# Kernel optimization log

Hardware: AMD Instinct MI355X
Metric: run time of the kernel (lower is better)

Reference implementation:

```python
import jax, jax.numpy as jnp
import numpy as np

HEAD_SIZE = 64
EPS_GN = 1e-5 * 8 * 8  # GroupNorm eps = 1e-5 * head_size_divisor**2


def rwkv7_scan(w_raw, q, k, v, a, b):
    """RWKV-7 'wind backstepping' linear recurrence.
    Inputs [B,T,H,N]. Per step (matching the CUDA kernel):
      decay = exp(-exp(w_raw)); sa = S @ a; S = S*decay + sa b^T + v k^T; y = S @ q
    State S is [B,H,N_value,N_key]."""
    decay = jnp.exp(-jnp.exp(w_raw))
    B, T, H, N = q.shape
    xs = tuple(jnp.moveaxis(t, 1, 0) for t in (decay, q, k, v, a, b))  # [T,B,H,N]
    S0 = jnp.zeros((B, H, N, N), q.dtype)

    def step(S, inp):
        d, qt, kt, vt, at, bt = inp
        sa = jnp.einsum('bhij,bhj->bhi', S, at)
        S = S * d[:, :, None, :] + sa[..., None] * bt[:, :, None, :] + vt[..., None] * kt[:, :, None, :]
        y = jnp.einsum('bhij,bhj->bhi', S, qt)
        return S, y

    _, ys = jax.lax.scan(step, S0, xs)
    return jnp.moveaxis(ys, 0, 1)  # [B,T,H,N]


def setup_inputs() -> dict:
    key = jax.random.key(0)
    B, T, C, H, N = 4, 960, 2048, 32, 64
    Dw, Da, Dv, Dg = 96, 96, 64, 256
    ks = iter(jax.random.split(key, 40))

    def nrm(shape, s=0.02):
        return jax.random.normal(next(ks), shape, jnp.float32) * s

    def uni(shape):
        return jax.random.uniform(next(ks), shape, jnp.float32)

    return dict(
        x=nrm((B, T, C), 1.0),
        v_first=nrm((B, T, C), 1.0),
        x_r=uni((1, 1, C)), x_w=uni((1, 1, C)), x_k=uni((1, 1, C)),
        x_v=uni((1, 1, C)), x_a=uni((1, 1, C)), x_g=uni((1, 1, C)),
        w0=jnp.linspace(-7.0, -2.0, C, dtype=jnp.float32).reshape(1, 1, C) + 0.5,
        w1=nrm((C, Dw)), w2=nrm((Dw, C)),
        a0=nrm((1, 1, C)), a1=nrm((C, Da)), a2=nrm((Da, C)),
        v0=jnp.ones((1, 1, C), jnp.float32), v1=nrm((C, Dv)), v2=nrm((Dv, C)),
        g1=nrm((C, Dg)), g2=nrm((Dg, C)),
        k_k=jnp.full((1, 1, C), 0.85, jnp.float32),
        k_a=jnp.ones((1, 1, C), jnp.float32),
        r_k=nrm((H, N)),
        Wr=nrm((C, C)), Wk=nrm((C, C)), Wv=nrm((C, C)), Wo=nrm((C, C)),
        ln_w=jnp.ones((C,), jnp.float32), ln_b=jnp.zeros((C,), jnp.float32),
    )


def reference(x, v_first, x_r, x_w, x_k, x_v, x_a, x_g,
              w0, w1, w2, a0, a1, a2, v0, v1, v2, g1, g2,
              k_k, k_a, r_k, Wr, Wk, Wv, Wo, ln_w, ln_b):
    B, T, C = x.shape
    H = C // HEAD_SIZE
    # time_shift: ZeroPad2d((0,0,1,-1)) == shift right by 1 along T with zero at t=0
    x_prev = jnp.pad(x, ((0, 0), (1, 0), (0, 0)))[:, :T]
    xx = x_prev - x
    xr = x + xx * x_r; xw = x + xx * x_w; xk = x + xx * x_k
    xv = x + xx * x_v; xa = x + xx * x_a; xg = x + xx * x_g

    r = xr @ Wr.T
    w = -jax.nn.softplus(-(w0 + jnp.tanh(xw @ w1) @ w2)) - 0.5
    k = xk @ Wk.T
    v = xv @ Wv.T
    # layer_id != 0: residual-value mixing with first layer's value
    v = v + (v_first - v) * jax.nn.sigmoid(v0 + (xv @ v1) @ v2)
    a = jax.nn.sigmoid(a0 + (xa @ a1) @ a2)
    g = jax.nn.sigmoid(xg @ g1) @ g2

    kk = (k * k_k).reshape(B, T, H, HEAD_SIZE)
    kk = kk / jnp.maximum(jnp.linalg.norm(kk, axis=-1, keepdims=True), 1e-12)  # F.normalize
    kk = kk.reshape(B, T, C)
    k = k * (1 + (a - 1) * k_a)

    hs = lambda t: t.reshape(B, T, H, HEAD_SIZE)
    y = rwkv7_scan(hs(w), hs(r), hs(k), hs(v), hs(-kk), hs(kk * a)).reshape(B, T, C)

    # GroupNorm(H groups over C)
    yg = y.reshape(B, T, H, HEAD_SIZE)
    mu = yg.mean(-1, keepdims=True)
    var = yg.var(-1, keepdims=True)
    y = ((yg - mu) / jnp.sqrt(var + EPS_GN)).reshape(B, T, C) * ln_w + ln_b

    y = y + ((hs(r) * hs(k) * r_k).sum(-1, keepdims=True) * hs(v)).reshape(B, T, C)
    return (y * g) @ Wo.T
```

## Files before the change

### kernel.cpp

```cpp
#include <hip/hip_runtime.h>
#include <stdint.h>

#define BDIM 4
#define TDIM 960
#define CDIM 2048
#define HDIM 32
#define NDIM 64
#define BT   (BDIM*TDIM)

typedef unsigned short u16;
typedef __attribute__((ext_vector_type(8))) short short8;
typedef __attribute__((ext_vector_type(4))) float f32x4;

__device__ __forceinline__ float b2f(u16 u){
  union{unsigned int i; float f;}x; x.i=((unsigned int)u)<<16; return x.f;
}
__device__ __forceinline__ u16 f2b(float f){
  union{float f; unsigned int i;}x; x.f=f;
  unsigned int r = x.i + 0x7fffu + ((x.i>>16)&1u);
  return (u16)(r>>16);
}
__device__ __forceinline__ void unpack8(uint4 p, float* o){
  o[0]=b2f((u16)(p.x&0xffff)); o[1]=b2f((u16)(p.x>>16));
  o[2]=b2f((u16)(p.y&0xffff)); o[3]=b2f((u16)(p.y>>16));
  o[4]=b2f((u16)(p.z&0xffff)); o[5]=b2f((u16)(p.z>>16));
  o[6]=b2f((u16)(p.w&0xffff)); o[7]=b2f((u16)(p.w>>16));
}
__device__ __forceinline__ uint4 pack8(const float* o){
  uint4 p;
  p.x = (unsigned)f2b(o[0]) | ((unsigned)f2b(o[1])<<16);
  p.y = (unsigned)f2b(o[2]) | ((unsigned)f2b(o[3])<<16);
  p.z = (unsigned)f2b(o[4]) | ((unsigned)f2b(o[5])<<16);
  p.w = (unsigned)f2b(o[6]) | ((unsigned)f2b(o[7])<<16);
  return p;
}
__device__ __forceinline__ void ld8f(const float* p, float* o){
  float4 a = *(const float4*)p;
  float4 b = *(const float4*)(p+4);
  o[0]=a.x;o[1]=a.y;o[2]=a.z;o[3]=a.w;o[4]=b.x;o[5]=b.y;o[6]=b.z;o[7]=b.w;
}
__device__ __forceinline__ float sigm(float x){ return 1.f/(1.f+expf(-x)); }
__device__ __forceinline__ void stc(float* p, float v){ *p = v; }
__device__ __forceinline__ void stc(u16* p, float v){ *p = f2b(v); }

__global__ __launch_bounds__(256) void cvt_kernel(const float* src, u16* dst){
  size_t i = ((size_t)blockIdx.x*256 + threadIdx.x)*8;
  float v[8]; ld8f(src+i, v);
  *(uint4*)(dst+i) = pack8(v);
}

struct TJob { const float* src; u16* dst; int R, Cs, DR, DC; };
struct TJobs8 { TJob j[8]; };

__global__ __launch_bounds__(256) void transpose_pad_kernel(TJobs8 jobs){
  TJob jb = jobs.j[blockIdx.z];
  int idx = blockIdx.x*256 + threadIdx.x;
  int total = jb.DR*jb.DC;
  if (idx >= total) return;
  int i = idx / jb.DC, k = idx % jb.DC;
  float v = 0.f;
  if (i < jb.Cs && k < jb.R) v = jb.src[(size_t)k*jb.Cs + i];
  jb.dst[idx] = f2b(v);
}

__global__ __launch_bounds__(256) void mix_kernel(
  const float* x,
  const float* cr, const float* cw, const float* ck,
  const float* cv, const float* ca, const float* cg,
  u16* mr, u16* mw, u16* mk, u16* mv, u16* ma, u16* mg)
{
  size_t tid = (size_t)blockIdx.x*256 + threadIdx.x;
  size_t base = tid*8;
  int c = (int)(base % CDIM);
  int row = (int)(base / CDIM);
  int t = row % TDIM;
  float xc[8], xp[8], xx[8], cf[8], o[8];
  ld8f(x+base, xc);
  if (t > 0) {
    ld8f(x+base-CDIM, xp);
  } else {
    for(int j=0;j<8;j++) xp[j]=0.f;
  }
  #pragma unroll
  for(int j=0;j<8;j++) xx[j]=xp[j]-xc[j];
#define DOMIX(CP, OP) do { ld8f(CP+c, cf); \
  _Pragma("unroll") for(int j=0;j<8;j++) o[j]=xc[j]+xx[j]*cf[j]; \
  *(uint4*)(OP+base)=pack8(o); } while(0)
  DOMIX(cr, mr); DOMIX(cw, mw); DOMIX(ck, mk);
  DOMIX(cv, mv); DOMIX(ca, ma); DOMIX(cg, mg);
#undef DOMIX
}

struct GemmJob {
  const u16* A; const u16* Bt; void* C;
  int nbm, nbn, K, lda, ldb, ldc;
};
struct GemmJobs { GemmJob j[4]; };

template<typename TC>
__global__ __launch_bounds__(256, 2) void gemm_bt_kernel(GemmJobs jobs){
  GemmJob jb = jobs.j[blockIdx.z];
  int bm = blockIdx.x % jb.nbm;
  int bn = blockIdx.x / jb.nbm;
  if (bn >= jb.nbn) return;
  __shared__ __attribute__((aligned(16))) u16 As[128*64];
  __shared__ __attribute__((aligned(16))) u16 Bs[128*64];
  int tid = threadIdx.x;
  int wave = tid>>6, lane = tid&63;
  int wr = wave>>1, wc = wave&1;
  f32x4 acc[4][4];
  #pragma unroll
  for(int i=0;i<4;i++)
    #pragma unroll
    for(int j=0;j<4;j++) acc[i][j] = (f32x4){0.f,0.f,0.f,0.f};
  const int rA0 = bm*128;
  const int rB0 = bn*128;
  int srow = (lane>>3);
  int scol = (lane&7)*8;
  for (int k0=0; k0<jb.K; k0+=64){
    #pragma unroll
    for (int it=0; it<4; ++it){
      int rr = wave*32 + it*8;
      const u16* gA = jb.A + (size_t)(rA0 + rr + srow)*jb.lda + (k0 + scol);
      __builtin_amdgcn_global_load_lds((const __attribute__((address_space(1))) void*)gA,
          (__attribute__((address_space(3))) void*)&As[rr*64], 16, 0, 0);
      const u16* gB = jb.Bt + (size_t)(rB0 + rr + srow)*jb.ldb + (k0 + scol);
      __builtin_amdgcn_global_load_lds((const __attribute__((address_space(1))) void*)gB,
          (__attribute__((address_space(3))) void*)&Bs[rr*64], 16, 0, 0);
    }
    __syncthreads();
    #pragma unroll
    for (int kc=0; kc<2; ++kc){
      short8 af[4], bfr[4];
      int ko = kc*32 + (lane>>4)*8;
      #pragma unroll
      for (int mi=0; mi<4; ++mi)
        af[mi] = *(const short8*)&As[(wr*64 + mi*16 + (lane&15))*64 + ko];
      #pragma unroll
      for (int ni=0; ni<4; ++ni)
        bfr[ni] = *(const short8*)&Bs[(wc*64 + ni*16 + (lane&15))*64 + ko];
      #pragma unroll
      for (int mi=0; mi<4; ++mi)
        #pragma unroll
        for (int ni=0; ni<4; ++ni)
          acc[mi][ni] = __builtin_amdgcn_mfma_f32_16x16x32_bf16(af[mi], bfr[ni], acc[mi][ni], 0, 0, 0);
    }
    __syncthreads();
  }
  TC* C = (TC*)jb.C;
  int cn = (lane&15);
  int rq = (lane>>4)*4;
  #pragma unroll
  for (int mi=0; mi<4; ++mi){
    #pragma unroll
    for (int ni=0; ni<4; ++ni){
      int col = rB0 + wc*64 + ni*16 + cn;
      int row = rA0 + wr*64 + mi*16 + rq;
      #pragma unroll
      for (int e=0; e<4; ++e)
        stc(&C[(size_t)(row+e)*jb.ldc + col], acc[mi][ni][e]);
    }
  }
}

__global__ __launch_bounds__(256) void act_kernel(u16* hw, u16* hg){
  int idx = blockIdx.x*256 + threadIdx.x;
  if (blockIdx.z==0){ if (idx < BT*128) hw[idx] = f2b(tanhf(b2f(hw[idx]))); }
  else              { if (idx < BT*256) hg[idx] = f2b(sigm(b2f(hg[idx]))); }
}

__global__ __launch_bounds__(256) void post_kernel(
  const u16* kbuf, const u16* vraw, const float* vfirst,
  const u16* wl, const u16* al, const u16* vl,
  const float* w0, const float* a0, const float* v0,
  const float* kkc, const float* kac,
  float* dout, u16* ks, u16* vs, u16* as_, u16* bs)
{
  int row = blockIdx.x, tid = threadIdx.x;
  int c = tid*8;
  size_t base = (size_t)row*CDIM + c;
  float kf[8], vr[8], vf[8], wlf[8], alf[8], vlf[8], w0f[8], a0f[8], v0f[8], kkf[8], kaf[8];
  unpack8(*(const uint4*)(kbuf+base), kf);
  unpack8(*(const uint4*)(vraw+base), vr);
  ld8f(vfirst+base, vf);
  unpack8(*(const uint4*)(wl+base), wlf);
  unpack8(*(const uint4*)(al+base), alf);
  unpack8(*(const uint4*)(vl+base), vlf);
  ld8f(w0+c, w0f);
  ld8f(a0+c, a0f);
  ld8f(v0+c, v0f);
  ld8f(kkc+c, kkf);
  ld8f(kac+c, kaf);
  float dv[8], av[8], vv[8], kkr[8], kfin[8], asv[8], bsv[8];
  float ssq = 0.f;
  #pragma unroll
  for (int j=0;j<8;j++){
    float wv = -log1pf(expf(-(w0f[j]+wlf[j]))) - 0.5f;
    dv[j]  = expf(-expf(wv));
    av[j]  = sigm(a0f[j]+alf[j]);
    vv[j]  = vr[j] + (vf[j]-vr[j])*sigm(v0f[j]+vlf[j]);
    kkr[j] = kf[j]*kkf[j];
    ssq   += kkr[j]*kkr[j];
    kfin[j]= kf[j]*(1.f + (av[j]-1.f)*kaf[j]);
  }
  ssq += __shfl_xor(ssq,1); ssq += __shfl_xor(ssq,2); ssq += __shfl_xor(ssq,4);
  float inv = 1.f/fmaxf(sqrtf(ssq), 1e-12f);
  #pragma unroll
  for (int j=0;j<8;j++){ float kkn = kkr[j]*inv; asv[j] = -kkn; bsv[j] = kkn*av[j]; }
  *(float4*)(dout+base)   = make_float4(dv[0],dv[1],dv[2],dv[3]);
  *(float4*)(dout+base+4) = make_float4(dv[4],dv[5],dv[6],dv[7]);
  *(uint4*)(ks+base)  = pack8(kfin);
  *(uint4*)(vs+base)  = pack8(vv);
  *(uint4*)(as_+base) = pack8(asv);
  *(uint4*)(bs+base)  = pack8(bsv);
}

__global__ __launch_bounds__(256) void scan_kernel(
  const float* decayp, const u16* qb, const u16* kb, const u16* vb,
  const u16* ab, const u16* bb, float* yb)
{
  const int DEC=0, QQ=512, KK=1024, AA=1536, BB=2048, VV=2560, BUF=2816;
  __shared__ float sb[2*2816];
  int blk = blockIdx.x;
  int b    = blk >> 6;
  int h    = (blk >> 1) & 31;
  int half = blk & 1;
  int tid = threadIdx.x;
  int jg = tid & 7;
  int ii = tid >> 3;
  int row = half*32 + ii;
  int lst = tid >> 5;
  int lc  = tid & 31;
  size_t hbase = ((size_t)b*TDIM)*CDIM + (size_t)h*NDIM;

  float S[8];
  #pragma unroll
  for (int e=0;e<8;e++) S[e]=0.f;

  float2 dreg; unsigned qreg, kreg, areg, breg; u16 vreg;
  auto load_group = [&](int t0){
    size_t g = hbase + (size_t)(t0+lst)*CDIM + lc*2;
    dreg = *(const float2*)(decayp + g);
    qreg = *(const unsigned*)(qb + g);
    kreg = *(const unsigned*)(kb + g);
    areg = *(const unsigned*)(ab + g);
    breg = *(const unsigned*)(bb + g);
    vreg = vb[hbase + (size_t)(t0+lst)*CDIM + half*32 + lc];
  };
  auto store_group = [&](int p){
    float* buf = &sb[p*BUF];
    *(float2*)&buf[DEC + lst*64 + lc*2] = dreg;
    *(float2*)&buf[QQ  + lst*64 + lc*2] = make_float2(b2f((u16)(qreg&0xffff)), b2f((u16)(qreg>>16)));
    *(float2*)&buf[KK  + lst*64 + lc*2] = make_float2(b2f((u16)(kreg&0xffff)), b2f((u16)(kreg>>16)));
    *(float2*)&buf[AA  + lst*64 + lc*2] = make_float2(b2f((u16)(areg&0xffff)), b2f((u16)(areg>>16)));
    *(float2*)&buf[BB  + lst*64 + lc*2] = make_float2(b2f((u16)(breg&0xffff)), b2f((u16)(breg>>16)));
    buf[VV + lst*32 + lc] = b2f(vreg);
  };

  load_group(0);
  store_group(0);
  __syncthreads();
  int p = 0;
  for (int g=0; g<120; ++g){
    if (g+1 < 120) load_group((g+1)*8);
    const float* buf = &sb[p*BUF];
    #pragma unroll
    for (int s=0; s<8; ++s){
      f32x4 a0 = *(const f32x4*)&buf[AA + s*64 + jg*8];
      f32x4 a1 = *(const f32x4*)&buf[AA + s*64 + jg*8 + 4];
      float sap = S[0]*a0[0]+S[1]*a0[1]+S[2]*a0[2]+S[3]*a0[3]
                + S[4]*a1[0]+S[5]*a1[1]+S[6]*a1[2]+S[7]*a1[3];
      sap += __shfl_xor(sap,1);
      sap += __shfl_xor(sap,2);
      sap += __shfl_xor(sap,4);
      f32x4 d0 = *(const f32x4*)&buf[DEC + s*64 + jg*8];
      f32x4 d1 = *(const f32x4*)&buf[DEC + s*64 + jg*8 + 4];
      f32x4 k0 = *(const f32x4*)&buf[KK + s*64 + jg*8];
      f32x4 k1 = *(const f32x4*)&buf[KK + s*64 + jg*8 + 4];
      f32x4 b0 = *(const f32x4*)&buf[BB + s*64 + jg*8];
      f32x4 b1 = *(const f32x4*)&buf[BB + s*64 + jg*8 + 4];
      f32x4 q0 = *(const f32x4*)&buf[QQ + s*64 + jg*8];
      f32x4 q1 = *(const f32x4*)&buf[QQ + s*64 + jg*8 + 4];
      float vi = buf[VV + s*32 + ii];
      float yp = 0.f;
      #pragma unroll
      for (int e=0;e<4;e++){
        S[e]   = S[e]*d0[e]   + sap*b0[e] + vi*k0[e];
        yp    += S[e]*q0[e];
        S[e+4] = S[e+4]*d1[e] + sap*b1[e] + vi*k1[e];
        yp    += S[e+4]*q1[e];
      }
      yp += __shfl_xor(yp,1);
      yp += __shfl_xor(yp,2);
      yp += __shfl_xor(yp,4);
      if (jg==0) yb[hbase + (size_t)(g*8+s)*CDIM + row] = yp;
    }
    if (g+1 < 120) store_group(p^1);
    __syncthreads();
    p ^= 1;
  }
}

__global__ __launch_bounds__(256) void final_kernel(
  const float* yb, const u16* rb, const u16* ks, const u16* vs,
  const float* rk, const float* lnw, const float* lnb, const u16* gl, u16* yg)
{
  int row = blockIdx.x, tid = threadIdx.x;
  int c = tid*8;
  size_t base = (size_t)row*CDIM + c;
  float y[8], rf[8], kf[8], vf[8], rkf[8], lw[8], lb[8], gf[8];
  ld8f(yb+base, y);
  unpack8(*(const uint4*)(rb+base), rf);
  unpack8(*(const uint4*)(ks+base), kf);
  unpack8(*(const uint4*)(vs+base), vf);
  ld8f(rk+c,  rkf);
  ld8f(lnw+c, lw);
  ld8f(lnb+c, lb);
  unpack8(*(const uint4*)(gl+base), gf);
  float sy=0.f, syy=0.f, coef=0.f;
  #pragma unroll
  for (int j=0;j<8;j++){ sy+=y[j]; syy+=y[j]*y[j]; coef += rf[j]*kf[j]*rkf[j]; }
  sy  += __shfl_xor(sy,1);  sy  += __shfl_xor(sy,2);  sy  += __shfl_xor(sy,4);
  syy += __shfl_xor(syy,1); syy += __shfl_xor(syy,2); syy += __shfl_xor(syy,4);
  coef+= __shfl_xor(coef,1);coef+= __shfl_xor(coef,2);coef+= __shfl_xor(coef,4);
  float mu  = sy*(1.f/64.f);
  float var = syy*(1.f/64.f) - mu*mu;
  float rs  = rsqrtf(var + 6.4e-4f);
  float o[8];
  #pragma unroll
  for (int j=0;j<8;j++)
    o[j] = (((y[j]-mu)*rs)*lw[j] + lb[j] + coef*vf[j]) * gf[j];
  *(uint4*)(yg+base) = pack8(o);
}

extern "C" void kernel_launch(void* const* d_in, const int* in_sizes, int n_in,
                              void* d_out, int out_size, void* d_ws, size_t ws_size,
                              hipStream_t stream)
{
  const float* x      = (const float*)d_in[0];
  const float* vfirst = (const float*)d_in[1];
  const float* c_r = (const float*)d_in[2];
  const float* c_w = (const float*)d_in[3];
  const float* c_k = (const float*)d_in[4];
  const float* c_v = (const float*)d_in[5];
  const float* c_a = (const float*)d_in[6];
  const float* c_g = (const float*)d_in[7];
  const float* w0i = (const float*)d_in[8];
  const float* w1i = (const float*)d_in[9];
  const float* w2i = (const float*)d_in[10];
  const float* a0i = (const float*)d_in[11];
  const float* a1i = (const float*)d_in[12];
  const float* a2i = (const float*)d_in[13];
  const float* v0i = (const float*)d_in[14];
  const float* v1i = (const float*)d_in[15];
  const float* v2i = (const float*)d_in[16];
  const float* g1i = (const float*)d_in[17];
  const float* g2i = (const float*)d_in[18];
  const float* kki = (const float*)d_in[19];
  const float* kai = (const float*)d_in[20];
  const float* rki = (const float*)d_in[21];
  const float* Wr  = (const float*)d_in[22];
  const float* Wk  = (const float*)d_in[23];
  const float* Wv  = (const float*)d_in[24];
  const float* Wo  = (const float*)d_in[25];
  const float* lnw = (const float*)d_in[26];
  const float* lnb = (const float*)d_in[27];

  char* ws = (char*)d_ws;
  const size_t S2 = (size_t)BT*CDIM*2;
  u16* MIXR = (u16*)(ws + 0*S2);
  u16* MIXW = (u16*)(ws + 1*S2);
  u16* MIXK = (u16*)(ws + 2*S2);
  u16* MIXV = (u16*)(ws + 3*S2);
  u16* MIXA = (u16*)(ws + 4*S2);
  u16* MIXG = (u16*)(ws + 5*S2);
  u16* RBUF = (u16*)(ws + 6*S2);
  u16* KBUF = (u16*)(ws + 7*S2);
  u16* VRAW = (u16*)(ws + 8*S2);
  char* WB = ws + 9*S2;
  u16* WSLOT = (u16*)WB;
  char* WT = WB + 8388608;
  u16* W1T = (u16*)(WT + 0);
  u16* A1T = (u16*)(WT + 524288);
  u16* V1T = (u16*)(WT + 1048576);
  u16* G1T = (u16*)(WT + 1572864);
  u16* W2T = (u16*)(WT + 2621440);
  u16* A2T = (u16*)(WT + 3145728);
  u16* V2T = (u16*)(WT + 3670016);
  u16* G2T = (u16*)(WT + 4194304);
  char* HB = WT + 5242880;
  u16* HW = (u16*)(HB + 0);
  u16* HA = (u16*)(HB + 983040);
  u16* HV = (u16*)(HB + 1966080);
  u16* HG = (u16*)(HB + 2949120);
  char* L2 = HB + 4915200;
  u16* WL = (u16*)(L2 + 0*S2);
  u16* AL = (u16*)(L2 + 1*S2);
  u16* VL = (u16*)(L2 + 2*S2);
  u16* GL = (u16*)(L2 + 3*S2);
  float* WDEC = (float*)(ws + 0*S2);
  u16* KS = (u16*)(ws + 2*S2);
  u16* VS = (u16*)(ws + 3*S2);
  u16* AS = (u16*)(ws + 4*S2);
  u16* BS = (u16*)(ws + 5*S2);
  float* YBUF = (float*)(L2 + 0*S2);
  u16* YG = (u16*)(L2 + 2*S2);
  (void)in_sizes; (void)n_in; (void)out_size; (void)ws_size;

  TJobs8 tj;
  tj.j[0] = (TJob){w1i, W1T, 2048,  96, 128, 2048};
  tj.j[1] = (TJob){a1i, A1T, 2048,  96, 128, 2048};
  tj.j[2] = (TJob){v1i, V1T, 2048,  64, 128, 2048};
  tj.j[3] = (TJob){g1i, G1T, 2048, 256, 256, 2048};
  tj.j[4] = (TJob){w2i, W2T,   96, 2048, 2048, 128};
  tj.j[5] = (TJob){a2i, A2T,   96, 2048, 2048, 128};
  tj.j[6] = (TJob){v2i, V2T,   64, 2048, 2048, 128};
  tj.j[7] = (TJob){g2i, G2T,  256, 2048, 2048, 256};
  transpose_pad_kernel<<<dim3(2048,1,8), 256, 0, stream>>>(tj);

  mix_kernel<<<dim3(BT*CDIM/8/256), 256, 0, stream>>>(
      x, c_r, c_w, c_k, c_v, c_a, c_g, MIXR, MIXW, MIXK, MIXV, MIXA, MIXG);

  {
    GemmJobs gj;
    cvt_kernel<<<dim3(2048), 256, 0, stream>>>(Wr, WSLOT);
    gj.j[0] = (GemmJob){MIXR, WSLOT, RBUF, 30, 16, 2048, 2048, 2048, 2048};
    gj.j[1] = gj.j[0]; gj.j[2] = gj.j[0]; gj.j[3] = gj.j[0];
    gemm_bt_kernel<u16><<<dim3(480,1,1), 256, 0, stream>>>(gj);
    cvt_kernel<<<dim3(2048), 256, 0, stream>>>(Wk, WSLOT);
    gj.j[0] = (GemmJob){MIXK, WSLOT, KBUF, 30, 16, 2048, 2048, 2048, 2048};
    gemm_bt_kernel<u16><<<dim3(480,1,1), 256, 0, stream>>>(gj);
    cvt_kernel<<<dim3(2048), 256, 0, stream>>>(Wv, WSLOT);
    gj.j[0] = (GemmJob){MIXV, WSLOT, VRAW, 30, 16, 2048, 2048, 2048, 2048};
    gemm_bt_kernel<u16><<<dim3(480,1,1), 256, 0, stream>>>(gj);
  }

  GemmJobs lj1;
  lj1.j[0] = (GemmJob){MIXW, W1T, HW, 30, 1, 2048, 2048, 2048, 128};
  lj1.j[1] = (GemmJob){MIXA, A1T, HA, 30, 1, 2048, 2048, 2048, 128};
  lj1.j[2] = (GemmJob){MIXV, V1T, HV, 30, 1, 2048, 2048, 2048, 128};
  lj1.j[3] = (GemmJob){MIXG, G1T, HG, 30, 2, 2048, 2048, 2048, 256};
  gemm_bt_kernel<u16><<<dim3(60,1,4), 256, 0, stream>>>(lj1);

  act_kernel<<<dim3(3840,1,2), 256, 0, stream>>>(HW, HG);

  GemmJobs lj2;
  lj2.j[0] = (GemmJob){HW, W2T, WL, 30, 16, 128, 128, 128, 2048};
  lj2.j[1] = (GemmJob){HA, A2T, AL, 30, 16, 128, 128, 128, 2048};
  lj2.j[2] = (GemmJob){HV, V2T, VL, 30, 16, 128, 128, 128, 2048};
  lj2.j[3] = (GemmJob){HG, G2T, GL, 30, 16, 256, 256, 256, 2048};
  gemm_bt_kernel<u16><<<dim3(480,1,4), 256, 0, stream>>>(lj2);

  post_kernel<<<dim3(BT), 256, 0, stream>>>(
      KBUF, VRAW, vfirst, WL, AL, VL, w0i, a0i, v0i, kki, kai,
      WDEC, KS, VS, AS, BS);

  scan_kernel<<<dim3(256), 256, 0, stream>>>(
      WDEC, RBUF, KS, VS, AS, BS, YBUF);

  final_kernel<<<dim3(BT), 256, 0, stream>>>(
      YBUF, RBUF, KS, VS, rki, lnw, lnb, GL, YG);

  cvt_kernel<<<dim3(2048), 256, 0, stream>>>(Wo, WSLOT);
  GemmJobs oj;
  oj.j[0] = (GemmJob){YG, WSLOT, d_out, 30, 16, 2048, 2048, 2048, 2048};
  oj.j[1] = oj.j[0]; oj.j[2] = oj.j[0]; oj.j[3] = oj.j[0];
  gemm_bt_kernel<float><<<dim3(480,1,1), 256, 0, stream>>>(oj);
}
```

Before: 908.2 us.

## Split scan state rows into quarters across 512 blocks with deferred y reduction

The RWKV-7 scan is now split four ways over value rows instead of two, giving 512 blocks of 256 threads, each thread holding 4 state elements instead of 8. Each row's dot products use 16 lanes, so the reductions gain an extra shuffle stage. The y reductions for the 8 timesteps in a group are batched after the inner loop, taking them off the serial per-step chain. The aim is more parallelism on a latency-bound recurrence, at the cost of redundantly loading each head's key-side vectors into LDS twice as many times.

```diff
diff --git a/kernel.cpp b/kernel.cpp
--- a/kernel.cpp
+++ b/kernel.cpp
@@ -215,29 +215,30 @@
   *(uint4*)(bs+base)  = pack8(bsv);
 }
 
-__global__ __launch_bounds__(256) void scan_kernel(
+__global__ __launch_bounds__(256, 2) void scan_kernel(
   const float* decayp, const u16* qb, const u16* kb, const u16* vb,
   const u16* ab, const u16* bb, float* yb)
 {
-  const int DEC=0, QQ=512, KK=1024, AA=1536, BB=2048, VV=2560, BUF=2816;
-  __shared__ float sb[2*2816];
+  const int DEC=0, QQ=512, KK=1024, AA=1536, BB=2048, VV=2560, BUF=2688;
+  __shared__ float sb[2*2688];
   int blk = blockIdx.x;
-  int b    = blk >> 6;
-  int h    = (blk >> 1) & 31;
-  int half = blk & 1;
+  int b    = blk >> 7;
+  int h    = (blk >> 2) & 31;
+  int qtr  = blk & 3;
   int tid = threadIdx.x;
-  int jg = tid & 7;
-  int ii = tid >> 3;
-  int row = half*32 + ii;
+  int jg = tid & 15;
+  int ii = tid >> 4;
+  int row0 = qtr*16;
+  int row = row0 + ii;
   int lst = tid >> 5;
   int lc  = tid & 31;
   size_t hbase = ((size_t)b*TDIM)*CDIM + (size_t)h*NDIM;
 
-  float S[8];
-  #pragma unroll
-  for (int e=0;e<8;e++) S[e]=0.f;
-
-  float2 dreg; unsigned qreg, kreg, areg, breg; u16 vreg;
+  float S[4];
+  #pragma unroll
+  for (int e=0;e<4;e++) S[e]=0.f;
+
+  float2 dreg; unsigned qreg, kreg, areg, breg; u16 vreg=0;
   auto load_group = [&](int t0){
     size_t g = hbase + (size_t)(t0+lst)*CDIM + lc*2;
     dreg = *(const float2*)(decayp + g);
@@ -245,7 +246,7 @@
     kreg = *(const unsigned*)(kb + g);
     areg = *(const unsigned*)(ab + g);
     breg = *(const unsigned*)(bb + g);
-    vreg = vb[hbase + (size_t)(t0+lst)*CDIM + half*32 + lc];
+    if (lc < 16) vreg = vb[hbase + (size_t)(t0+lst)*CDIM + row0 + lc];
   };
   auto store_group = [&](int p){
     float* buf = &sb[p*BUF];
@@ -254,7 +255,7 @@
     *(float2*)&buf[KK  + lst*64 + lc*2] = make_float2(b2f((u16)(kreg&0xffff)), b2f((u16)(kreg>>16)));
     *(float2*)&buf[AA  + lst*64 + lc*2] = make_float2(b2f((u16)(areg&0xffff)), b2f((u16)(areg>>16)));
     *(float2*)&buf[BB  + lst*64 + lc*2] = make_float2(b2f((u16)(breg&0xffff)), b2f((u16)(breg>>16)));
-    buf[VV + lst*32 + lc] = b2f(vreg);
+    if (lc < 16) buf[VV + lst*16 + lc] = b2f(vreg);
   };
 
   load_group(0);
@@ -264,36 +265,37 @@
   for (int g=0; g<120; ++g){
     if (g+1 < 120) load_group((g+1)*8);
     const float* buf = &sb[p*BUF];
+    float yp[8];
     #pragma unroll
     for (int s=0; s<8; ++s){
-      f32x4 a0 = *(const f32x4*)&buf[AA + s*64 + jg*8];
-      f32x4 a1 = *(const f32x4*)&buf[AA + s*64 + jg*8 + 4];
-      float sap = S[0]*a0[0]+S[1]*a0[1]+S[2]*a0[2]+S[3]*a0[3]
-                + S[4]*a1[0]+S[5]*a1[1]+S[6]*a1[2]+S[7]*a1[3];
+      f32x4 a0 = *(const f32x4*)&buf[AA + s*64 + jg*4];
+      float sap = (S[0]*a0[0] + S[1]*a0[1]) + (S[2]*a0[2] + S[3]*a0[3]);
       sap += __shfl_xor(sap,1);
       sap += __shfl_xor(sap,2);
       sap += __shfl_xor(sap,4);
-      f32x4 d0 = *(const f32x4*)&buf[DEC + s*64 + jg*8];
-      f32x4 d1 = *(const f32x4*)&buf[DEC + s*64 + jg*8 + 4];
-      f32x4 k0 = *(const f32x4*)&buf[KK + s*64 + jg*8];
-      f32x4 k1 = *(const f32x4*)&buf[KK + s*64 + jg*8 + 4];
-      f32x4 b0 = *(const f32x4*)&buf[BB + s*64 + jg*8];
-      f32x4 b1 = *(const f32x4*)&buf[BB + s*64 + jg*8 + 4];
-      f32x4 q0 = *(const f32x4*)&buf[QQ + s*64 + jg*8];
-      f32x4 q1 = *(const f32x4*)&buf[QQ + s*64 + jg*8 + 4];
-      float vi = buf[VV + s*32 + ii];
-      float yp = 0.f;
-      #pragma unroll
-      for (int e=0;e<4;e++){
-        S[e]   = S[e]*d0[e]   + sap*b0[e] + vi*k0[e];
-        yp    += S[e]*q0[e];
-        S[e+4] = S[e+4]*d1[e] + sap*b1[e] + vi*k1[e];
-        yp    += S[e+4]*q1[e];
-      }
-      yp += __shfl_xor(yp,1);
-      yp += __shfl_xor(yp,2);
-      yp += __shfl_xor(yp,4);
-      if (jg==0) yb[hbase + (size_t)(g*8+s)*CDIM + row] = yp;
+      sap += __shfl_xor(sap,8);
+      f32x4 d0 = *(const f32x4*)&buf[DEC + s*64 + jg*4];
+      f32x4 k0 = *(const f32x4*)&buf[KK  + s*64 + jg*4];
+      f32x4 b0 = *(const f32x4*)&buf[BB  + s*64 + jg*4];
+      f32x4 q0 = *(const f32x4*)&buf[QQ  + s*64 + jg*4];
+      float vi = buf[VV + s*16 + ii];
+      #pragma unroll
+      for (int e=0;e<4;e++)
+        S[e] = S[e]*d0[e] + sap*b0[e] + vi*k0[e];
+      yp[s] = (S[0]*q0[0] + S[1]*q0[1]) + (S[2]*q0[2] + S[3]*q0[3]);
+    }
+    #pragma unroll
+    for (int s=0; s<8; ++s){
+      yp[s] += __shfl_xor(yp[s],1);
+      yp[s] += __shfl_xor(yp[s],2);
+      yp[s] += __shfl_xor(yp[s],4);
+      yp[s] += __shfl_xor(yp[s],8);
+    }
+    if (jg < 8){
+      float out = 0.f;
+      #pragma unroll
+      for (int s=0; s<8; ++s) if (jg==s) out = yp[s];
+      yb[hbase + (size_t)(g*8+jg)*CDIM + row] = out;
     }
     if (g+1 < 120) store_group(p^1);
     __syncthreads();
@@ -455,7 +457,7 @@
       KBUF, VRAW, vfirst, WL, AL, VL, w0i, a0i, v0i, kki, kai,
       WDEC, KS, VS, AS, BS);
 
-  scan_kernel<<<dim3(256), 256, 0, stream>>>(
+  scan_kernel<<<dim3(512), 256, 0, stream>>>(
       WDEC, RBUF, KS, VS, AS, BS, YBUF);
 
   final_kernel<<<dim3(BT), 256, 0, stream>>>(
```

Result: faster. 889.1 us (-2.1%).
